# Kernel tuning notes

Hardware: AMD Instinct MI355X
Metric: run time of the kernel (lower is better)

The kernel has to match this reference:

```python
import jax, jax.numpy as jnp
from jax import lax
import numpy as np

# Reconstructed utils constants
PSZ = 24     # patch size
KS = 3       # kernel size of generated conv kernels
FILTERS = 9  # channels / number of generated filters
STRIDE = 8   # conv stride inside KGL


def setup_inputs() -> dict:
    key = jax.random.key(0)
    k1, k2, k3 = jax.random.split(key, 3)
    B, H, W = 8, 768, 768
    x = jax.random.normal(k1, (B, H, W, FILTERS), dtype=jnp.float32)
    conv_w = jax.random.normal(k2, (KS, KS, FILTERS, 9), dtype=jnp.float32) * 0.05  # HWIO
    conv_b = jnp.zeros((9,), dtype=jnp.float32)
    dense_w = jax.random.normal(k3, (FILTERS, FILTERS * FILTERS), dtype=jnp.float32) * 0.05
    dense_b = jnp.zeros((FILTERS * FILTERS,), dtype=jnp.float32)
    return {"x": x, "conv_w": conv_w, "conv_b": conv_b, "dense_w": dense_w, "dense_b": dense_b}


def _clip_by_norm(t, axes, clip_norm=1.0):
    # tf.clip_by_norm: t * clip_norm / max(||t||_2_over_axes, clip_norm)
    l2 = jnp.sqrt(jnp.sum(t * t, axis=axes, keepdims=True))
    return t * (clip_norm / jnp.maximum(l2, clip_norm))


def reference(x, conv_w, conv_b, dense_w, dense_b):
    B, H, W, C = x.shape
    p1, p2 = H // PSZ, W // PSZ
    N = p1 * p2
    # tf.image.extract_patches layout: [B, p1, p2, PSZ*PSZ*C] with patch flattened row-major (row, col, chan)
    patches = x.reshape(B, p1, PSZ, p2, PSZ, C).transpose(0, 1, 3, 2, 4, 5)  # [B,p1,p2,PSZ,PSZ,C]
    # RAW reshape to (N, B, PSZ, PSZ, C) exactly as the TF code does (buffer reinterpretation)
    patches = patches.reshape(N, B, PSZ, PSZ, C)
    flat = patches.reshape(N * B, PSZ, PSZ, C)

    # --- W_G1: per-patch conv kernel generation ---
    conv_out = lax.conv_general_dilated(
        flat, conv_w, window_strides=(STRIDE, STRIDE), padding="SAME",
        dimension_numbers=("NHWC", "HWIO", "NHWC")) + conv_b  # [N*B, 3, 3, 9]
    wg1 = conv_out.reshape(N * B, KS, KS, FILTERS, 1)
    wg1 = _clip_by_norm(wg1, axes=(1, 2))                      # norm over (KS, KS) dims
    wg1 = wg1.reshape(N, B, KS, KS, FILTERS, 1)

    # --- W_G2: per-patch 1x1 mixing kernel via GAP + Dense ---
    gap = flat.mean(axis=(1, 2))                               # [N*B, C]
    d = gap @ dense_w + dense_b                                # [N*B, FILTERS^2]
    wg2 = d.reshape(N * B, 1, 1, FILTERS, FILTERS)
    wg2 = _clip_by_norm(wg2, axes=(1, 2, 3))
    wg2 = wg2.reshape(N, B, 1, 1, FILTERS, FILTERS)
    return wg1, wg2
```

## Files before the change

### kernel.cpp

```cpp
#include <hip/hip_runtime.h>


#define PSZ 24
#define NCH 9
#define HW 768
#define PATCH_ELEMS (PSZ*PSZ*NCH)
#define PATCH_V4 1296
#define NPIX (PSZ*PSZ)
#define ROWF (PSZ*NCH)
#define ROWV4 54
#define XROWF (HW*NCH)
#define OUT1_OFF 0
#define OUT2_OFF 663552

__device__ inline void async_load16(const void* g, void* l) {
    __builtin_amdgcn_global_load_lds(
        (const __attribute__((address_space(1))) void*)g,
        (__attribute__((address_space(3))) void*)l, 16, 0, 0);
}

__global__ __launch_bounds__(256) void kgl_kernel(
    const float* __restrict__ x,
    const float* __restrict__ conv_w,
    const float* __restrict__ conv_b,
    const float* __restrict__ dense_w,
    const float* __restrict__ dense_b,
    float* __restrict__ out)
{
    __shared__ __align__(16) float patch[PATCH_ELEMS];
    __shared__ __align__(16) float cw[732];
    __shared__ __align__(16) float colsum[ROWF];
    __shared__ float co_s[81];
    __shared__ float d_s[81];
    __shared__ float gap_s[NCH];
    __shared__ float sc1[NCH];
    __shared__ float sc2[NCH];

    const int j   = blockIdx.x;
    const int b   = j >> 10;
    const int rem = j & 1023;
    const int pi  = rem >> 5;
    const int pj  = rem & 31;
    const int tid = threadIdx.x;

    if (tid < 182) {
        reinterpret_cast<float4*>(cw)[tid] =
            reinterpret_cast<const float4*>(conv_w)[tid];
    } else if (tid == 182) {
        cw[728] = conv_w[728];
    }

    const size_t base = ((size_t)(b*HW + pi*PSZ) * HW + (size_t)pj*PSZ) * NCH;
    const float* gbase = x + base;
    #pragma unroll
    for (int it = 0; it < 6; ++it) {
        int e4 = tid + it*256;
        if (e4 < PATCH_V4) {
            int r = e4 / ROWV4;
            int t = e4 - r*ROWV4;
            async_load16(gbase + (size_t)r*XROWF + t*4, &patch[e4*4]);
        }
    }
    __syncthreads();

    if (tid < 81) {
        const int oy = tid / 27;
        const int ox = (tid / 9) % 3;
        const int oc = tid % 9;
        float acc = conv_b[oc];
        #pragma unroll
        for (int ky = 0; ky < 3; ++ky) {
            #pragma unroll
            for (int kx = 0; kx < 3; ++kx) {
                const float* pp = &patch[(oy*8+ky)*ROWF + (ox*8+kx)*NCH];
                const float* ww = &cw[(ky*3+kx)*81 + oc];
                #pragma unroll
                for (int ic = 0; ic < 9; ++ic) acc += pp[ic] * ww[ic*9];
            }
        }
        co_s[tid] = acc;
    } else if (tid >= 128 && tid < 128+ROWV4) {
        const int k = tid - 128;
        const float4* pv = reinterpret_cast<const float4*>(patch);
        float4 acc = pv[k];
        #pragma unroll
        for (int r = 1; r < PSZ; ++r) {
            float4 v = pv[r*ROWV4 + k];
            acc.x += v.x; acc.y += v.y; acc.z += v.z; acc.w += v.w;
        }
        reinterpret_cast<float4*>(colsum)[k] = acc;
    }
    __syncthreads();

    if (tid < NCH) {
        float n2 = 0.f;
        #pragma unroll
        for (int s9 = 0; s9 < 9; ++s9) {
            float v = co_s[s9*9 + tid];
            n2 += v*v;
        }
        sc1[tid] = 1.0f / fmaxf(sqrtf(n2), 1.0f);
    } else if (tid >= 128 && tid < 128+NCH) {
        const int c = tid - 128;
        float s = 0.f;
        #pragma unroll
        for (int i = 0; i < PSZ; ++i) s += colsum[c + NCH*i];
        gap_s[c] = s * (1.0f / (float)NPIX);
    }
    __syncthreads();

    if (tid < 81) {
        float acc = dense_b[tid];
        #pragma unroll
        for (int c = 0; c < NCH; ++c) acc += gap_s[c] * dense_w[c*81 + tid];
        d_s[tid] = acc;

        out[OUT1_OFF + (size_t)j*81 + tid] = co_s[tid] * sc1[tid % 9];
    }
    __syncthreads();

    if (tid < NCH) {
        float n2 = 0.f;
        #pragma unroll
        for (int a = 0; a < 9; ++a) {
            float v = d_s[a*9 + tid];
            n2 += v*v;
        }
        sc2[tid] = 1.0f / fmaxf(sqrtf(n2), 1.0f);
    }
    __syncthreads();

    if (tid < 81) {
        out[OUT2_OFF + (size_t)j*81 + tid] = d_s[tid] * sc2[tid % 9];
    }
}

extern "C" void kernel_launch(void* const* d_in, const int* in_sizes, int n_in,
                              void* d_out, int out_size, void* d_ws, size_t ws_size,
                              hipStream_t stream) {
    const float* x       = (const float*)d_in[0];
    const float* conv_w  = (const float*)d_in[1];
    const float* conv_b  = (const float*)d_in[2];
    const float* dense_w = (const float*)d_in[3];
    const float* dense_b = (const float*)d_in[4];
    float* out = (float*)d_out;

    kgl_kernel<<<8192, 256, 0, stream>>>(x, conv_w, conv_b, dense_w, dense_b, out);
}
```

Measured before the change: 241.3 us.

## Specialize waves: compute conv from global while other waves stream patch to LDS

The 256-thread block is split by wave. Waves 0-1 load the conv weights into per-wave LDS copies and compute the strided 3x3 conv directly from global memory. Waves 2-3 issue all async patch loads into LDS and then do the column reduction for the global average, split into two half-height partial sums. Each output thread now computes its own clip-norm scale, which removes two __syncthreads phases. The intent is to overlap the conv with the patch transfer and shorten the serial barrier chain. The cost is that only two waves now issue the patch loads, and the conv windows are read from global a second time.

```diff
diff --git a/kernel.cpp b/kernel.cpp
--- a/kernel.cpp
+++ b/kernel.cpp
@@ -10,7 +10,6 @@
 #define ROWF (PSZ*NCH)
 #define ROWV4 54
 #define XROWF (HW*NCH)
-#define OUT1_OFF 0
 #define OUT2_OFF 663552
 
 __device__ inline void async_load16(const void* g, void* l) {
@@ -28,13 +27,14 @@
     float* __restrict__ out)
 {
     __shared__ __align__(16) float patch[PATCH_ELEMS];
-    __shared__ __align__(16) float cw[732];
-    __shared__ __align__(16) float colsum[ROWF];
+    __shared__ __align__(16) float cwA[732];
+    __shared__ __align__(16) float cwB[732];
+    __shared__ __align__(16) float colA[ROWF];
+    __shared__ __align__(16) float colB[ROWF];
+    __shared__ float gapA[NCH];
+    __shared__ float gapB[NCH];
     __shared__ float co_s[81];
     __shared__ float d_s[81];
-    __shared__ float gap_s[NCH];
-    __shared__ float sc1[NCH];
-    __shared__ float sc2[NCH];
 
     const int j   = blockIdx.x;
     const int b   = j >> 10;
@@ -43,95 +43,115 @@
     const int pj  = rem & 31;
     const int tid = threadIdx.x;
 
-    if (tid < 182) {
-        reinterpret_cast<float4*>(cw)[tid] =
-            reinterpret_cast<const float4*>(conv_w)[tid];
-    } else if (tid == 182) {
-        cw[728] = conv_w[728];
-    }
+    const size_t base = ((size_t)(b*HW + pi*PSZ) * HW + (size_t)pj*PSZ) * NCH;
 
-    const size_t base = ((size_t)(b*HW + pi*PSZ) * HW + (size_t)pj*PSZ) * NCH;
-    const float* gbase = x + base;
-    #pragma unroll
-    for (int it = 0; it < 6; ++it) {
-        int e4 = tid + it*256;
-        if (e4 < PATCH_V4) {
-            int r = e4 / ROWV4;
-            int t = e4 - r*ROWV4;
-            async_load16(gbase + (size_t)r*XROWF + t*4, &patch[e4*4]);
+    float conv_acc = 0.f;
+
+    if (tid < 128) {
+        float* cw = (tid < 64) ? cwA : cwB;
+        const int lane = tid & 63;
+        #pragma unroll
+        for (int i = 0; i < 3; ++i) {
+            int e = lane + i*64;
+            if (e < 182)
+                reinterpret_cast<float4*>(cw)[e] =
+                    reinterpret_cast<const float4*>(conv_w)[e];
+        }
+        if (lane == 0) cw[728] = conv_w[728];
+
+        if (tid < 81) {
+            const int oy = tid / 27;
+            const int ox = (tid / 9) % 3;
+            const int oc = tid % 9;
+            float acc = conv_b[oc];
+            #pragma unroll
+            for (int ky = 0; ky < 3; ++ky) {
+                const float* gp = x + base + (size_t)(oy*8+ky)*XROWF + (size_t)(ox*8)*NCH;
+                const float4* gp4 = reinterpret_cast<const float4*>(gp);
+                float pv[27];
+                #pragma unroll
+                for (int q = 0; q < 6; ++q) {
+                    float4 v = gp4[q];
+                    pv[q*4+0] = v.x; pv[q*4+1] = v.y; pv[q*4+2] = v.z; pv[q*4+3] = v.w;
+                }
+                pv[24] = gp[24]; pv[25] = gp[25]; pv[26] = gp[26];
+                #pragma unroll
+                for (int kx = 0; kx < 3; ++kx) {
+                    #pragma unroll
+                    for (int ic = 0; ic < 9; ++ic)
+                        acc += pv[kx*9+ic] * cw[(ky*3+kx)*81 + ic*9 + oc];
+                }
+            }
+            co_s[tid] = acc;
+            conv_acc = acc;
+        }
+    } else {
+        const float* gbase = x + base;
+        #pragma unroll
+        for (int it = 0; it < 11; ++it) {
+            int e4 = (tid - 128) + it*128;
+            if (e4 < PATCH_V4) {
+                int r = e4 / ROWV4;
+                int t = e4 - r*ROWV4;
+                async_load16(gbase + (size_t)r*XROWF + t*4, &patch[e4*4]);
+            }
         }
     }
     __syncthreads();
 
     if (tid < 81) {
-        const int oy = tid / 27;
-        const int ox = (tid / 9) % 3;
         const int oc = tid % 9;
-        float acc = conv_b[oc];
-        #pragma unroll
-        for (int ky = 0; ky < 3; ++ky) {
-            #pragma unroll
-            for (int kx = 0; kx < 3; ++kx) {
-                const float* pp = &patch[(oy*8+ky)*ROWF + (ox*8+kx)*NCH];
-                const float* ww = &cw[(ky*3+kx)*81 + oc];
-                #pragma unroll
-                for (int ic = 0; ic < 9; ++ic) acc += pp[ic] * ww[ic*9];
-            }
-        }
-        co_s[tid] = acc;
-    } else if (tid >= 128 && tid < 128+ROWV4) {
-        const int k = tid - 128;
-        const float4* pv = reinterpret_cast<const float4*>(patch);
-        float4 acc = pv[k];
-        #pragma unroll
-        for (int r = 1; r < PSZ; ++r) {
-            float4 v = pv[r*ROWV4 + k];
-            acc.x += v.x; acc.y += v.y; acc.z += v.z; acc.w += v.w;
-        }
-        reinterpret_cast<float4*>(colsum)[k] = acc;
-    }
-    __syncthreads();
-
-    if (tid < NCH) {
         float n2 = 0.f;
         #pragma unroll
-        for (int s9 = 0; s9 < 9; ++s9) {
-            float v = co_s[s9*9 + tid];
+        for (int s = 0; s < 9; ++s) {
+            float v = co_s[s*9 + oc];
             n2 += v*v;
         }
-        sc1[tid] = 1.0f / fmaxf(sqrtf(n2), 1.0f);
-    } else if (tid >= 128 && tid < 128+NCH) {
-        const int c = tid - 128;
-        float s = 0.f;
-        #pragma unroll
-        for (int i = 0; i < PSZ; ++i) s += colsum[c + NCH*i];
-        gap_s[c] = s * (1.0f / (float)NPIX);
+        float sc = 1.0f / fmaxf(sqrtf(n2), 1.0f);
+        out[(size_t)j*81 + tid] = conv_acc * sc;
+    } else if (tid >= 128) {
+        const int w  = (tid >= 192) ? 1 : 0;
+        const int k  = tid & 63;
+        float* col   = w ? colB : colA;
+        const int r0 = w ? 12 : 0;
+        if (k < ROWV4) {
+            const float4* pv = reinterpret_cast<const float4*>(patch);
+            float4 acc = pv[r0*ROWV4 + k];
+            #pragma unroll
+            for (int r = 1; r < 12; ++r) {
+                float4 v = pv[(r0+r)*ROWV4 + k];
+                acc.x += v.x; acc.y += v.y; acc.z += v.z; acc.w += v.w;
+            }
+            reinterpret_cast<float4*>(col)[k] = acc;
+        }
+        if (k < NCH) {
+            float s = 0.f;
+            #pragma unroll
+            for (int i = 0; i < 24; ++i) s += col[k + NCH*i];
+            if (w) gapB[k] = s; else gapA[k] = s;
+        }
     }
     __syncthreads();
 
     if (tid < 81) {
-        float acc = dense_b[tid];
+        float d = dense_b[tid];
         #pragma unroll
-        for (int c = 0; c < NCH; ++c) acc += gap_s[c] * dense_w[c*81 + tid];
-        d_s[tid] = acc;
-
-        out[OUT1_OFF + (size_t)j*81 + tid] = co_s[tid] * sc1[tid % 9];
-    }
-    __syncthreads();
-
-    if (tid < NCH) {
-        float n2 = 0.f;
-        #pragma unroll
-        for (int a = 0; a < 9; ++a) {
-            float v = d_s[a*9 + tid];
-            n2 += v*v;
-        }
-        sc2[tid] = 1.0f / fmaxf(sqrtf(n2), 1.0f);
+        for (int c = 0; c < NCH; ++c)
+            d += (gapA[c] + gapB[c]) * (1.0f/(float)NPIX) * dense_w[c*81 + tid];
+        d_s[tid] = d;
     }
     __syncthreads();
 
     if (tid < 81) {
-        out[OUT2_OFF + (size_t)j*81 + tid] = d_s[tid] * sc2[tid % 9];
+        const int bc = tid % 9;
+        float n2 = 0.f;
+        #pragma unroll
+        for (int a = 0; a < 9; ++a) {
+            float v = d_s[a*9 + bc];
+            n2 += v*v;
+        }
+        float sc = 1.0f / fmaxf(sqrtf(n2), 1.0f);
+        out[OUT2_OFF + (size_t)j*81 + tid] = d_s[tid] * sc;
     }
 }
 
```

New measurement: 241.5 us. About the same (+0.1%).
